# Kernel optimization log

Measured on AMD Instinct MI355X. Metric: run time of the kernel, lower is better.

The kernel has to match this reference:

```python
import jax, jax.numpy as jnp
import numpy as np

N_NODES = 50000
IN_CH, HID_CH, OUT_CH = 128, 128, 16
N_EDGES = 800000


def setup_inputs() -> dict:
    key = jax.random.key(0)
    ks = jax.random.split(key, 10)
    def lin_w(k, fan_in, fan_out):
        bound = 1.0 / np.sqrt(fan_in)
        return jax.random.uniform(k, (fan_in, fan_out), jnp.float32, -bound, bound)
    inp = {
        'x': jax.random.normal(ks[0], (N_NODES, IN_CH), jnp.float32),
        'edge_index': jax.random.randint(ks[1], (2, N_EDGES), 0, N_NODES, jnp.int64),
        # SAGEConv l/r weights: lin_l (neighbor aggregate, with bias), lin_r (root, no bias)
        'W1_l': lin_w(ks[2], IN_CH, HID_CH), 'b1': jnp.zeros((HID_CH,), jnp.float32),
        'W1_r': lin_w(ks[3], IN_CH, HID_CH),
        'W2_l': lin_w(ks[4], HID_CH, HID_CH), 'b2': jnp.zeros((HID_CH,), jnp.float32),
        'W2_r': lin_w(ks[5], HID_CH, HID_CH),
        'W3_l': lin_w(ks[6], HID_CH, HID_CH), 'b3': jnp.zeros((HID_CH,), jnp.float32),
        'W3_r': lin_w(ks[7], HID_CH, HID_CH),
        'W_lin': lin_w(ks[8], HID_CH, OUT_CH), 'b_lin': jnp.zeros((OUT_CH,), jnp.float32),
    }
    return inp


def _sage_conv(x, src, dst, W_l, b_l, W_r, n_nodes):
    # mean aggregation of source-node features at destination nodes
    msg_sum = jax.ops.segment_sum(x[src], dst, num_segments=n_nodes)  # [N, d]
    deg = jax.ops.segment_sum(jnp.ones((src.shape[0],), x.dtype), dst, num_segments=n_nodes)
    mean = msg_sum / jnp.maximum(deg, 1.0)[:, None]
    return mean @ W_l + b_l + x @ W_r


def reference(x, edge_index, W1_l, b1, W1_r, W2_l, b2, W2_r, W3_l, b3, W3_r, W_lin, b_lin):
    src, dst = edge_index[0], edge_index[1]
    n = x.shape[0]
    h = jax.nn.relu(_sage_conv(x, src, dst, W1_l, b1, W1_r, n))
    h = jax.nn.relu(_sage_conv(h, src, dst, W2_l, b2, W2_r, n))
    # dropout is identity in eval mode
    h = jax.nn.relu(_sage_conv(h, src, dst, W3_l, b3, W3_r, n))
    return h @ W_lin + b_lin
```

## Files before the change

### kernel.cpp

```cpp
#include <hip/hip_runtime.h>


typedef short bf16x8 __attribute__((ext_vector_type(8)));
typedef float f32x4 __attribute__((ext_vector_type(4)));

__device__ __forceinline__ float bf16_to_f32(unsigned int lo16) {
  unsigned int u = lo16 << 16;
  return __builtin_bit_cast(float, u);
}
__device__ __forceinline__ unsigned short f32_to_bf16(float f) {
  unsigned int u = __builtin_bit_cast(unsigned int, f);
  unsigned int r = (u + 0x7FFFu + ((u >> 16) & 1u)) >> 16;
  return (unsigned short)r;
}

__device__ __forceinline__ void gload_lds16(const void* g, void* lds_base) {
  __builtin_amdgcn_global_load_lds(
      (__attribute__((address_space(1))) unsigned int*)(uintptr_t)g,
      (__attribute__((address_space(3))) unsigned int*)(unsigned int)(uintptr_t)lds_base,
      16, 0, 0);
}

__global__ void k_zero_i32(int* __restrict__ p, int n) {
  int i = blockIdx.x * blockDim.x + threadIdx.x;
  if (i < n) p[i] = 0;
}

__global__ __launch_bounds__(256) void k_split(const float* __restrict__ in,
                                               unsigned short* __restrict__ hi,
                                               unsigned short* __restrict__ lo, int n4) {
  int i = blockIdx.x * blockDim.x + threadIdx.x;
  if (i < n4) {
    float4 v = *reinterpret_cast<const float4*>(&in[(size_t)i * 4]);
    ushort4 h, l;
    h.x = f32_to_bf16(v.x); l.x = f32_to_bf16(v.x - bf16_to_f32(h.x));
    h.y = f32_to_bf16(v.y); l.y = f32_to_bf16(v.y - bf16_to_f32(h.y));
    h.z = f32_to_bf16(v.z); l.z = f32_to_bf16(v.z - bf16_to_f32(h.z));
    h.w = f32_to_bf16(v.w); l.w = f32_to_bf16(v.w - bf16_to_f32(h.w));
    *reinterpret_cast<ushort4*>(&hi[(size_t)i * 4]) = h;
    *reinterpret_cast<ushort4*>(&lo[(size_t)i * 4]) = l;
  }
}

__global__ __launch_bounds__(256) void k_prep_w(const float* __restrict__ Wl,
                                                const float* __restrict__ Wr,
                                                unsigned short* __restrict__ Whi,
                                                unsigned short* __restrict__ Wlo) {
  int n = blockIdx.x, k = threadIdx.x;
  float v = (k < 128) ? Wl[(size_t)k * 128 + n] : Wr[(size_t)(k - 128) * 128 + n];
  unsigned short h = f32_to_bf16(v);
  Whi[(size_t)n * 256 + k] = h;
  Wlo[(size_t)n * 256 + k] = f32_to_bf16(v - bf16_to_f32(h));
}

__global__ void k_detect(const int* __restrict__ ei, int* __restrict__ flag) {
  int t = threadIdx.x;
  int any = 0;
  for (int i = t; i < 1024; i += 256)
    if (ei[2 * i + 1] != 0) any = 1;
  if (any) atomicOr(flag, 1);
}

__device__ __forceinline__ int load_src(const int* ei, int E, int i, int is32) {
  return is32 ? ei[i] : ei[2 * i];
}
__device__ __forceinline__ int load_dst(const int* ei, int E, int i, int is32) {
  return is32 ? ei[E + i] : ei[2 * E + 2 * i];
}

__global__ __launch_bounds__(256) void k_count(const int* __restrict__ ei,
                                               const int* __restrict__ flag,
                                               int* __restrict__ deg,
                                               int* __restrict__ erank, int E) {
  int i = blockIdx.x * blockDim.x + threadIdx.x;
  if (i < E) {
    int is32 = *flag;
    erank[i] = atomicAdd(&deg[load_dst(ei, E, i, is32)], 1);
  }
}

__global__ __launch_bounds__(256) void k_scan1(const int* __restrict__ deg,
                                               int* __restrict__ bsum, int N) {
  __shared__ int s[256];
  int t = threadIdx.x;
  int base = blockIdx.x * 1024 + t * 4;
  int v = 0;
#pragma unroll
  for (int j = 0; j < 4; ++j) {
    int i = base + j;
    v += (i < N) ? deg[i] : 0;
  }
  s[t] = v;
  __syncthreads();
  for (int off = 128; off > 0; off >>= 1) {
    if (t < off) s[t] += s[t + off];
    __syncthreads();
  }
  if (t == 0) bsum[blockIdx.x] = s[0];
}

__global__ __launch_bounds__(1024) void k_scan2(int* __restrict__ bsum,
                                                int* __restrict__ row_ptr,
                                                int nb, int N) {
  __shared__ int s[1024];
  int t = threadIdx.x;
  int v = (t < nb) ? bsum[t] : 0;
  s[t] = v;
  __syncthreads();
  for (int off = 1; off < 1024; off <<= 1) {
    int add = (t >= off) ? s[t - off] : 0;
    __syncthreads();
    s[t] += add;
    __syncthreads();
  }
  if (t < nb) bsum[t] = s[t] - v;
  if (t == 1023) row_ptr[N] = s[1023];
}

__global__ __launch_bounds__(256) void k_scan3(const int* __restrict__ deg,
                                               const int* __restrict__ bsum,
                                               int* __restrict__ row_ptr,
                                               float* __restrict__ inv_deg, int N) {
  __shared__ int s[256];
  int t = threadIdx.x;
  int base = blockIdx.x * 1024 + t * 4;
  int v[4];
  int sum = 0;
#pragma unroll
  for (int j = 0; j < 4; ++j) {
    int i = base + j;
    v[j] = (i < N) ? deg[i] : 0;
    sum += v[j];
  }
  s[t] = sum;
  __syncthreads();
  for (int off = 1; off < 256; off <<= 1) {
    int add = (t >= off) ? s[t - off] : 0;
    __syncthreads();
    s[t] += add;
    __syncthreads();
  }
  int excl = s[t] - sum + bsum[blockIdx.x];
#pragma unroll
  for (int j = 0; j < 4; ++j) {
    int i = base + j;
    if (i < N) {
      row_ptr[i] = excl;
      inv_deg[i] = 1.0f / (float)((v[j] > 1) ? v[j] : 1);
      excl += v[j];
    }
  }
}

__global__ __launch_bounds__(256) void k_fill(const int* __restrict__ ei,
                                              const int* __restrict__ flag,
                                              const int* __restrict__ row_ptr,
                                              const int* __restrict__ erank,
                                              int* __restrict__ col_idx, int E) {
  int i = blockIdx.x * blockDim.x + threadIdx.x;
  if (i < E) {
    int is32 = *flag;
    int d = load_dst(ei, E, i, is32);
    int s = load_src(ei, E, i, is32);
    col_idx[row_ptr[d] + erank[i]] = s;
  }
}

__global__ __launch_bounds__(256) void k_aggregate(const unsigned short* __restrict__ Xhi,
                                                   const int* __restrict__ row_ptr,
                                                   const int* __restrict__ col_idx,
                                                   const float* __restrict__ inv_deg,
                                                   unsigned int* __restrict__ Mhi,
                                                   unsigned int* __restrict__ Mlo, int N) {
  int gw = (int)((blockIdx.x * blockDim.x + threadIdx.x) >> 6);
  int lane = threadIdx.x & 63;
  if (gw >= N) return;
  int s = row_ptr[gw], e = row_ptr[gw + 1];
  const unsigned int* Xp =
      reinterpret_cast<const unsigned int*>(Xhi) + lane;
  float ax[8], ay[8];
#pragma unroll
  for (int q = 0; q < 8; ++q) { ax[q] = 0.f; ay[q] = 0.f; }
  int j = s;
  for (; j + 8 <= e; j += 8) {
    unsigned int v[8];
#pragma unroll
    for (int q = 0; q < 8; ++q) v[q] = Xp[(size_t)col_idx[j + q] * 64];
#pragma unroll
    for (int q = 0; q < 8; ++q) {
      ax[q] += bf16_to_f32(v[q] & 0xFFFFu);
      ay[q] += bf16_to_f32(v[q] >> 16);
    }
  }
  for (; j + 4 <= e; j += 4) {
    unsigned int v[4];
#pragma unroll
    for (int q = 0; q < 4; ++q) v[q] = Xp[(size_t)col_idx[j + q] * 64];
#pragma unroll
    for (int q = 0; q < 4; ++q) {
      ax[q] += bf16_to_f32(v[q] & 0xFFFFu);
      ay[q] += bf16_to_f32(v[q] >> 16);
    }
  }
  for (; j < e; ++j) {
    unsigned int v = Xp[(size_t)col_idx[j] * 64];
    ax[0] += bf16_to_f32(v & 0xFFFFu);
    ay[0] += bf16_to_f32(v >> 16);
  }
  float inv = inv_deg[gw];
  float rx = ((ax[0] + ax[1]) + (ax[2] + ax[3])) + ((ax[4] + ax[5]) + (ax[6] + ax[7]));
  float ry = ((ay[0] + ay[1]) + (ay[2] + ay[3])) + ((ay[4] + ay[5]) + (ay[6] + ay[7]));
  rx *= inv;
  ry *= inv;
  unsigned int hx = f32_to_bf16(rx), hy = f32_to_bf16(ry);
  unsigned int lx = f32_to_bf16(rx - bf16_to_f32(hx));
  unsigned int ly = f32_to_bf16(ry - bf16_to_f32(hy));
  Mhi[(size_t)gw * 64 + lane] = hx | (hy << 16);
  Mlo[(size_t)gw * 64 + lane] = lx | (ly << 16);
}

__global__ __launch_bounds__(256) void k_mfma_gemm(
    const unsigned short* __restrict__ A1hi, const unsigned short* __restrict__ A1lo,
    const unsigned short* __restrict__ A2hi, const unsigned short* __restrict__ A2lo,
    const unsigned short* __restrict__ Whi, const unsigned short* __restrict__ Wlo,
    const float* __restrict__ bias,
    unsigned short* __restrict__ Ohi, unsigned short* __restrict__ Olo, int N) {
  __shared__ unsigned short sAhi[2][128 * 32], sAlo[2][128 * 32];
  __shared__ unsigned short sBhi[2][128 * 32], sBlo[2][128 * 32];
  int t = threadIdx.x;
  int lane = t & 63;
  int w = t >> 6;
  int wr = (w >> 1) * 64, wc = (w & 1) * 64;
  int block_row = blockIdx.x * 128;

  f32x4 acc[4][4];
#pragma unroll
  for (int m = 0; m < 4; ++m)
#pragma unroll
    for (int n = 0; n < 4; ++n) acc[m][n] = f32x4{0.f, 0.f, 0.f, 0.f};

  int kg = lane & 3;
  int rr = lane >> 2;
  int fr = lane & 15;
  int fkb = (lane >> 4) * 16;

  auto stage = [&](int kt, int b) {
    const unsigned short* gsrc;
    unsigned short* lbase;
    int isA = (w < 2);
    if (w == 0) { gsrc = (kt < 4) ? A1hi : A2hi; lbase = sAhi[b]; }
    else if (w == 1) { gsrc = (kt < 4) ? A1lo : A2lo; lbase = sAlo[b]; }
    else if (w == 2) { gsrc = Whi; lbase = sBhi[b]; }
    else { gsrc = Wlo; lbase = sBlo[b]; }
#pragma unroll
    for (int c = 0; c < 8; ++c) {
      int idx = c * 16 + rr;
      const char* src;
      if (isA) {
        int rg = block_row + idx;
        if (rg > N - 1) rg = N - 1;
        src = (const char*)gsrc + (size_t)rg * 256 + (kt & 3) * 64 + kg * 16;
      } else {
        src = (const char*)gsrc + (size_t)idx * 512 + kt * 64 + kg * 16;
      }
      gload_lds16(src, (char*)lbase + c * 1024);
    }
  };

  stage(0, 0);
  __syncthreads();

  for (int kt = 0; kt < 8; ++kt) {
    int cur = kt & 1;
    if (kt < 7) stage(kt + 1, cur ^ 1);
    bf16x8 a_hi[4], a_lo[4], b_hi[4], b_lo[4];
#pragma unroll
    for (int m = 0; m < 4; ++m) {
      int row = wr + m * 16 + fr;
      a_hi[m] = *reinterpret_cast<const bf16x8*>((const char*)sAhi[cur] + row * 64 + fkb);
      a_lo[m] = *reinterpret_cast<const bf16x8*>((const char*)sAlo[cur] + row * 64 + fkb);
    }
#pragma unroll
    for (int n = 0; n < 4; ++n) {
      int col = wc + n * 16 + fr;
      b_hi[n] = *reinterpret_cast<const bf16x8*>((const char*)sBhi[cur] + col * 64 + fkb);
      b_lo[n] = *reinterpret_cast<const bf16x8*>((const char*)sBlo[cur] + col * 64 + fkb);
    }
#pragma unroll
    for (int m = 0; m < 4; ++m)
#pragma unroll
      for (int n = 0; n < 4; ++n) {
        acc[m][n] = __builtin_amdgcn_mfma_f32_16x16x32_bf16(a_hi[m], b_hi[n], acc[m][n], 0, 0, 0);
        acc[m][n] = __builtin_amdgcn_mfma_f32_16x16x32_bf16(a_hi[m], b_lo[n], acc[m][n], 0, 0, 0);
        acc[m][n] = __builtin_amdgcn_mfma_f32_16x16x32_bf16(a_lo[m], b_hi[n], acc[m][n], 0, 0, 0);
      }
    __syncthreads();
  }

  float bv[4];
#pragma unroll
  for (int n = 0; n < 4; ++n) bv[n] = bias[wc + n * 16 + (lane & 15)];
#pragma unroll
  for (int m = 0; m < 4; ++m) {
#pragma unroll
    for (int n = 0; n < 4; ++n) {
#pragma unroll
      for (int j = 0; j < 4; ++j) {
        int row_l = wr + m * 16 + (lane >> 4) * 4 + j;
        int g = block_row + row_l;
        if (g < N) {
          int col = wc + n * 16 + (lane & 15);
          float v = fmaxf(acc[m][n][j] + bv[n], 0.f);
          unsigned short h = f32_to_bf16(v);
          Ohi[(size_t)g * 128 + col] = h;
          Olo[(size_t)g * 128 + col] = f32_to_bf16(v - bf16_to_f32(h));
        }
      }
    }
  }
}

__global__ __launch_bounds__(256) void k_final(const unsigned short* __restrict__ Hhi,
                                               const unsigned short* __restrict__ Hlo,
                                               const float* __restrict__ W,
                                               const float* __restrict__ b,
                                               float* __restrict__ Out, int N) {
  __shared__ float sH[16][128];
  __shared__ float sW[128][16];
  __shared__ float sb[16];
  int t = threadIdx.x;
  int node0 = blockIdx.x * 16;
  {
    int row = t >> 4, q = t & 15;
    int g = node0 + row;
    if (g < N) {
      uint4 hv = *reinterpret_cast<const uint4*>(&Hhi[(size_t)g * 128 + q * 8]);
      uint4 lv = *reinterpret_cast<const uint4*>(&Hlo[(size_t)g * 128 + q * 8]);
      const unsigned short* hp = (const unsigned short*)&hv;
      const unsigned short* lp = (const unsigned short*)&lv;
#pragma unroll
      for (int e = 0; e < 8; ++e)
        sH[row][q * 8 + e] = bf16_to_f32(hp[e]) + bf16_to_f32(lp[e]);
    } else {
#pragma unroll
      for (int e = 0; e < 8; ++e) sH[row][q * 8 + e] = 0.f;
    }
  }
  for (int j = t; j < 512; j += 256) {
    int row = j >> 2, q = j & 3;
    *reinterpret_cast<float4*>(&sW[row][q * 4]) =
        *reinterpret_cast<const float4*>(&W[(size_t)row * 16 + q * 4]);
  }
  if (t < 16) sb[t] = b[t];
  __syncthreads();
  int node = t >> 4, col = t & 15;
  float acc = sb[col];
#pragma unroll 8
  for (int k = 0; k < 128; ++k) acc = fmaf(sH[node][k], sW[k][col], acc);
  int g = node0 + node;
  if (g < N) Out[(size_t)g * 16 + col] = acc;
}

extern "C" void kernel_launch(void* const* d_in, const int* in_sizes, int n_in,
                              void* d_out, int out_size, void* d_ws, size_t ws_size,
                              hipStream_t stream) {
  if (n_in < 13) return;
  const float* x = (const float*)d_in[0];
  const int* ei = (const int*)d_in[1];
  const float* W1l = (const float*)d_in[2];
  const float* b1 = (const float*)d_in[3];
  const float* W1r = (const float*)d_in[4];
  const float* W2l = (const float*)d_in[5];
  const float* b2 = (const float*)d_in[6];
  const float* W2r = (const float*)d_in[7];
  const float* W3l = (const float*)d_in[8];
  const float* b3 = (const float*)d_in[9];
  const float* W3r = (const float*)d_in[10];
  const float* Wlin = (const float*)d_in[11];
  const float* blin = (const float*)d_in[12];
  float* out = (float*)d_out;

  const int N = in_sizes[0] / 128;
  const int E = in_sizes[1] / 2;

  char* w = (char*)d_ws;
  size_t off = 0;
  auto alloc = [&](size_t bytes) -> void* {
    off = (off + 255) & ~(size_t)255;
    void* p = (void*)(w + off);
    off += bytes;
    return p;
  };
  size_t actB = (size_t)N * 128 * 2;
  unsigned short* Xhi = (unsigned short*)alloc(actB);
  unsigned short* Xlo = (unsigned short*)alloc(actB);
  unsigned short* Ahi = (unsigned short*)alloc(actB);
  unsigned short* Alo = (unsigned short*)alloc(actB);
  unsigned short* Mhi = (unsigned short*)alloc(actB);
  unsigned short* Mlo = (unsigned short*)alloc(actB);
  unsigned short* Wt[6];
  for (int i = 0; i < 6; ++i) Wt[i] = (unsigned short*)alloc(128 * 256 * 2);
  int* deg = (int*)alloc((size_t)N * 4);
  int* row_ptr = (int*)alloc((size_t)(N + 1) * 4);
  int* col_idx = (int*)alloc((size_t)E * 4);
  int* erank = (int*)alloc((size_t)E * 4);
  float* invdeg = (float*)alloc((size_t)N * 4);
  int* flag = (int*)alloc(4);
  int* bsum = (int*)alloc((size_t)1024 * 4);
  (void)ws_size;

  const int nbScan = (N + 1023) / 1024;

  k_zero_i32<<<(N + 255) / 256, 256, 0, stream>>>(deg, N);
  k_zero_i32<<<1, 256, 0, stream>>>(flag, 1);
  k_detect<<<1, 256, 0, stream>>>(ei, flag);
  k_count<<<(E + 255) / 256, 256, 0, stream>>>(ei, flag, deg, erank, E);
  k_split<<<(N * 32 + 255) / 256, 256, 0, stream>>>(x, Xhi, Xlo, N * 32);
  k_prep_w<<<128, 256, 0, stream>>>(W1l, W1r, Wt[0], Wt[1]);
  k_prep_w<<<128, 256, 0, stream>>>(W2l, W2r, Wt[2], Wt[3]);
  k_prep_w<<<128, 256, 0, stream>>>(W3l, W3r, Wt[4], Wt[5]);
  k_scan1<<<nbScan, 256, 0, stream>>>(deg, bsum, N);
  k_scan2<<<1, 1024, 0, stream>>>(bsum, row_ptr, nbScan, N);
  k_scan3<<<nbScan, 256, 0, stream>>>(deg, bsum, row_ptr, invdeg, N);
  k_fill<<<(E + 255) / 256, 256, 0, stream>>>(ei, flag, row_ptr, erank, col_idx, E);

  int aggBlocks = (N * 64 + 255) / 256;
  int gemmBlocks = (N + 127) / 128;

  k_aggregate<<<aggBlocks, 256, 0, stream>>>(Xhi, row_ptr, col_idx, invdeg,
                                             (unsigned int*)Mhi, (unsigned int*)Mlo, N);
  k_mfma_gemm<<<gemmBlocks, 256, 0, stream>>>(Mhi, Mlo, Xhi, Xlo, Wt[0], Wt[1], b1,
                                              Ahi, Alo, N);
  k_aggregate<<<aggBlocks, 256, 0, stream>>>(Ahi, row_ptr, col_idx, invdeg,
                                             (unsigned int*)Mhi, (unsigned int*)Mlo, N);
  k_mfma_gemm<<<gemmBlocks, 256, 0, stream>>>(Mhi, Mlo, Ahi, Alo, Wt[2], Wt[3], b2,
                                              Xhi, Xlo, N);
  k_aggregate<<<aggBlocks, 256, 0, stream>>>(Xhi, row_ptr, col_idx, invdeg,
                                             (unsigned int*)Mhi, (unsigned int*)Mlo, N);
  k_mfma_gemm<<<gemmBlocks, 256, 0, stream>>>(Mhi, Mlo, Xhi, Xlo, Wt[4], Wt[5], b3,
                                              Ahi, Alo, N);
  k_final<<<(N + 15) / 16, 256, 0, stream>>>(Ahi, Alo, Wlin, blin, out, N);
}
```

Baseline: 269.8 us.

## Slice aggregation by feature quarter so XCD-local L2 caches hold a feature slice

Adds an aggregation kernel where each block handles a 64-byte feature slice (one of four) for 16 nodes. A 16-lane group gathers that slice per neighbor, and slice = blockIdx & 3 maps the slice to interleaved XCDs. The aim is to shrink the gathered working set each XCD's L2 must hold, improving cache hit rates for random neighbor gathers. In exchange each gather touches only 64 bytes per row, giving narrower memory transactions and four times the row_ptr/col_idx reads. The new kernel is used for layers 1 and 3; layer 2 keeps the old kernel.

```diff
diff --git a/kernel.cpp b/kernel.cpp
--- a/kernel.cpp
+++ b/kernel.cpp
@@ -217,6 +217,51 @@
   unsigned int ly = f32_to_bf16(ry - bf16_to_f32(hy));
   Mhi[(size_t)gw * 64 + lane] = hx | (hy << 16);
   Mlo[(size_t)gw * 64 + lane] = lx | (ly << 16);
+}
+
+__global__ __launch_bounds__(256) void k_agg_xcd(const unsigned short* __restrict__ Xhi,
+                                                 const int* __restrict__ row_ptr,
+                                                 const int* __restrict__ col_idx,
+                                                 const float* __restrict__ inv_deg,
+                                                 unsigned int* __restrict__ Mhi,
+                                                 unsigned int* __restrict__ Mlo, int N) {
+  int b = blockIdx.x;
+  int slice = b & 3;
+  int chunk = b >> 2;
+  int t = threadIdx.x;
+  int wave = t >> 6, lane = t & 63;
+  int grp = lane >> 4, sl = lane & 15;
+  int node = chunk * 16 + wave * 4 + grp;
+  if (node >= N) return;
+  int s = row_ptr[node], e = row_ptr[node + 1];
+  const unsigned int* Xp =
+      reinterpret_cast<const unsigned int*>(Xhi) + slice * 16 + sl;
+  float ax0 = 0.f, ay0 = 0.f, ax1 = 0.f, ay1 = 0.f;
+  float ax2 = 0.f, ay2 = 0.f, ax3 = 0.f, ay3 = 0.f;
+  int j = s;
+  for (; j + 4 <= e; j += 4) {
+    unsigned int v0 = Xp[(size_t)col_idx[j] * 64];
+    unsigned int v1 = Xp[(size_t)col_idx[j + 1] * 64];
+    unsigned int v2 = Xp[(size_t)col_idx[j + 2] * 64];
+    unsigned int v3 = Xp[(size_t)col_idx[j + 3] * 64];
+    ax0 += bf16_to_f32(v0 & 0xFFFFu); ay0 += bf16_to_f32(v0 >> 16);
+    ax1 += bf16_to_f32(v1 & 0xFFFFu); ay1 += bf16_to_f32(v1 >> 16);
+    ax2 += bf16_to_f32(v2 & 0xFFFFu); ay2 += bf16_to_f32(v2 >> 16);
+    ax3 += bf16_to_f32(v3 & 0xFFFFu); ay3 += bf16_to_f32(v3 >> 16);
+  }
+  for (; j < e; ++j) {
+    unsigned int v = Xp[(size_t)col_idx[j] * 64];
+    ax0 += bf16_to_f32(v & 0xFFFFu);
+    ay0 += bf16_to_f32(v >> 16);
+  }
+  float inv = inv_deg[node];
+  float rx = ((ax0 + ax1) + (ax2 + ax3)) * inv;
+  float ry = ((ay0 + ay1) + (ay2 + ay3)) * inv;
+  unsigned int hx = f32_to_bf16(rx), hy = f32_to_bf16(ry);
+  unsigned int lx = f32_to_bf16(rx - bf16_to_f32(hx));
+  unsigned int ly = f32_to_bf16(ry - bf16_to_f32(hy));
+  Mhi[(size_t)node * 64 + slice * 16 + sl] = hx | (hy << 16);
+  Mlo[(size_t)node * 64 + slice * 16 + sl] = lx | (ly << 16);
 }
 
 __global__ __launch_bounds__(256) void k_mfma_gemm(
@@ -425,9 +470,10 @@
   k_fill<<<(E + 255) / 256, 256, 0, stream>>>(ei, flag, row_ptr, erank, col_idx, E);
 
   int aggBlocks = (N * 64 + 255) / 256;
+  int sliceBlocks = ((N + 15) / 16) * 4;
   int gemmBlocks = (N + 127) / 128;
 
-  k_aggregate<<<aggBlocks, 256, 0, stream>>>(Xhi, row_ptr, col_idx, invdeg,
+  k_agg_xcd<<<sliceBlocks, 256, 0, stream>>>(Xhi, row_ptr, col_idx, invdeg,
                                              (unsigned int*)Mhi, (unsigned int*)Mlo, N);
   k_mfma_gemm<<<gemmBlocks, 256, 0, stream>>>(Mhi, Mlo, Xhi, Xlo, Wt[0], Wt[1], b1,
                                               Ahi, Alo, N);
@@ -435,7 +481,7 @@
                                              (unsigned int*)Mhi, (unsigned int*)Mlo, N);
   k_mfma_gemm<<<gemmBlocks, 256, 0, stream>>>(Mhi, Mlo, Ahi, Alo, Wt[2], Wt[3], b2,
                                               Xhi, Xlo, N);
-  k_aggregate<<<aggBlocks, 256, 0, stream>>>(Xhi, row_ptr, col_idx, invdeg,
+  k_agg_xcd<<<sliceBlocks, 256, 0, stream>>>(Xhi, row_ptr, col_idx, invdeg,
                                              (unsigned int*)Mhi, (unsigned int*)Mlo, N);
   k_mfma_gemm<<<gemmBlocks, 256, 0, stream>>>(Mhi, Mlo, Xhi, Xlo, Wt[4], Wt[5], b3,
                                               Ahi, Alo, N);
```

After: 303.0 us. 1.12x slower.

## Fuse final linear into last SAGE GEMM and merge weight prep launches

Applied to the files above, without the earlier changes.

Fuses the third layer's MFMA GEMM with the output linear projection: the ReLU'd hidden tile is split into bf16 hi/lo in LDS and multiplied by Wlin via MFMA, so the 50000x128 activation is never written to or re-read from global memory. It also merges the three weight-prep launches into one and folds the flag zeroing into the detect kernel, cutting the number of kernel launches. The final projection now uses split-bf16 MFMA instead of fp32 FMA, a small change in numerics, and the fused kernel does extra per-block work loading Wlin.

```diff
diff --git a/kernel.cpp b/kernel.cpp
--- a/kernel.cpp
+++ b/kernel.cpp
@@ -42,11 +42,20 @@
   }
 }
 
-__global__ __launch_bounds__(256) void k_prep_w(const float* __restrict__ Wl,
-                                                const float* __restrict__ Wr,
-                                                unsigned short* __restrict__ Whi,
-                                                unsigned short* __restrict__ Wlo) {
-  int n = blockIdx.x, k = threadIdx.x;
+__global__ __launch_bounds__(256) void k_prep_w3(
+    const float* __restrict__ W1l, const float* __restrict__ W1r,
+    const float* __restrict__ W2l, const float* __restrict__ W2r,
+    const float* __restrict__ W3l, const float* __restrict__ W3r,
+    unsigned short* __restrict__ Whi1, unsigned short* __restrict__ Wlo1,
+    unsigned short* __restrict__ Whi2, unsigned short* __restrict__ Wlo2,
+    unsigned short* __restrict__ Whi3, unsigned short* __restrict__ Wlo3) {
+  int layer = blockIdx.x >> 7;
+  int n = blockIdx.x & 127;
+  int k = threadIdx.x;
+  const float* Wl = (layer == 0) ? W1l : (layer == 1) ? W2l : W3l;
+  const float* Wr = (layer == 0) ? W1r : (layer == 1) ? W2r : W3r;
+  unsigned short* Whi = (layer == 0) ? Whi1 : (layer == 1) ? Whi2 : Whi3;
+  unsigned short* Wlo = (layer == 0) ? Wlo1 : (layer == 1) ? Wlo2 : Wlo3;
   float v = (k < 128) ? Wl[(size_t)k * 128 + n] : Wr[(size_t)(k - 128) * 128 + n];
   unsigned short h = f32_to_bf16(v);
   Whi[(size_t)n * 256 + k] = h;
@@ -55,6 +64,8 @@
 
 __global__ void k_detect(const int* __restrict__ ei, int* __restrict__ flag) {
   int t = threadIdx.x;
+  if (t == 0) *flag = 0;
+  __syncthreads();
   int any = 0;
   for (int i = t; i < 1024; i += 256)
     if (ei[2 * i + 1] != 0) any = 1;
@@ -320,45 +331,146 @@
   }
 }
 
-__global__ __launch_bounds__(256) void k_final(const unsigned short* __restrict__ Hhi,
-                                               const unsigned short* __restrict__ Hlo,
-                                               const float* __restrict__ W,
-                                               const float* __restrict__ b,
-                                               float* __restrict__ Out, int N) {
-  __shared__ float sH[16][128];
-  __shared__ float sW[128][16];
-  __shared__ float sb[16];
+__global__ __launch_bounds__(256) void k_mfma_gemm_final(
+    const unsigned short* __restrict__ A1hi, const unsigned short* __restrict__ A1lo,
+    const unsigned short* __restrict__ A2hi, const unsigned short* __restrict__ A2lo,
+    const unsigned short* __restrict__ Whi, const unsigned short* __restrict__ Wlo,
+    const float* __restrict__ bias,
+    const float* __restrict__ Wlin, const float* __restrict__ blin,
+    float* __restrict__ Out, int N) {
+  __shared__ unsigned short smem[32768];
   int t = threadIdx.x;
-  int node0 = blockIdx.x * 16;
-  {
-    int row = t >> 4, q = t & 15;
-    int g = node0 + row;
-    if (g < N) {
-      uint4 hv = *reinterpret_cast<const uint4*>(&Hhi[(size_t)g * 128 + q * 8]);
-      uint4 lv = *reinterpret_cast<const uint4*>(&Hlo[(size_t)g * 128 + q * 8]);
-      const unsigned short* hp = (const unsigned short*)&hv;
-      const unsigned short* lp = (const unsigned short*)&lv;
-#pragma unroll
-      for (int e = 0; e < 8; ++e)
-        sH[row][q * 8 + e] = bf16_to_f32(hp[e]) + bf16_to_f32(lp[e]);
-    } else {
-#pragma unroll
-      for (int e = 0; e < 8; ++e) sH[row][q * 8 + e] = 0.f;
-    }
-  }
-  for (int j = t; j < 512; j += 256) {
-    int row = j >> 2, q = j & 3;
-    *reinterpret_cast<float4*>(&sW[row][q * 4]) =
-        *reinterpret_cast<const float4*>(&W[(size_t)row * 16 + q * 4]);
-  }
-  if (t < 16) sb[t] = b[t];
-  __syncthreads();
-  int node = t >> 4, col = t & 15;
-  float acc = sb[col];
-#pragma unroll 8
-  for (int k = 0; k < 128; ++k) acc = fmaf(sH[node][k], sW[k][col], acc);
-  int g = node0 + node;
-  if (g < N) Out[(size_t)g * 16 + col] = acc;
+  int lane = t & 63;
+  int w = t >> 6;
+  int wr = (w >> 1) * 64, wc = (w & 1) * 64;
+  int block_row = blockIdx.x * 128;
+
+  int kg = lane & 3;
+  int rr = lane >> 2;
+  int fr = lane & 15;
+  int fkb = (lane >> 4) * 16;
+  int ke = (lane >> 4) * 8;
+  int colw = lane & 15;
+
+  bf16x8 wbh[4], wbl[4];
+#pragma unroll
+  for (int ks = 0; ks < 4; ++ks) {
+#pragma unroll
+    for (int e = 0; e < 8; ++e) {
+      float wv = Wlin[(size_t)(ks * 32 + ke + e) * 16 + colw];
+      unsigned short h = f32_to_bf16(wv);
+      wbh[ks][e] = (short)h;
+      wbl[ks][e] = (short)f32_to_bf16(wv - bf16_to_f32(h));
+    }
+  }
+
+  f32x4 acc[4][4];
+#pragma unroll
+  for (int m = 0; m < 4; ++m)
+#pragma unroll
+    for (int n = 0; n < 4; ++n) acc[m][n] = f32x4{0.f, 0.f, 0.f, 0.f};
+
+  auto sAhi = [&](int b) { return smem + b * 4096; };
+  auto sAlo = [&](int b) { return smem + 8192 + b * 4096; };
+  auto sBhi = [&](int b) { return smem + 16384 + b * 4096; };
+  auto sBlo = [&](int b) { return smem + 24576 + b * 4096; };
+
+  auto stage = [&](int kt, int b) {
+    const unsigned short* gsrc;
+    unsigned short* lbase;
+    int isA = (w < 2);
+    if (w == 0) { gsrc = (kt < 4) ? A1hi : A2hi; lbase = sAhi(b); }
+    else if (w == 1) { gsrc = (kt < 4) ? A1lo : A2lo; lbase = sAlo(b); }
+    else if (w == 2) { gsrc = Whi; lbase = sBhi(b); }
+    else { gsrc = Wlo; lbase = sBlo(b); }
+#pragma unroll
+    for (int c = 0; c < 8; ++c) {
+      int idx = c * 16 + rr;
+      const char* src;
+      if (isA) {
+        int rg = block_row + idx;
+        if (rg > N - 1) rg = N - 1;
+        src = (const char*)gsrc + (size_t)rg * 256 + (kt & 3) * 64 + kg * 16;
+      } else {
+        src = (const char*)gsrc + (size_t)idx * 512 + kt * 64 + kg * 16;
+      }
+      gload_lds16(src, (char*)lbase + c * 1024);
+    }
+  };
+
+  stage(0, 0);
+  __syncthreads();
+
+  for (int kt = 0; kt < 8; ++kt) {
+    int cur = kt & 1;
+    if (kt < 7) stage(kt + 1, cur ^ 1);
+    bf16x8 a_hi[4], a_lo[4], b_hi[4], b_lo[4];
+#pragma unroll
+    for (int m = 0; m < 4; ++m) {
+      int row = wr + m * 16 + fr;
+      a_hi[m] = *reinterpret_cast<const bf16x8*>((const char*)sAhi(cur) + row * 64 + fkb);
+      a_lo[m] = *reinterpret_cast<const bf16x8*>((const char*)sAlo(cur) + row * 64 + fkb);
+    }
+#pragma unroll
+    for (int n = 0; n < 4; ++n) {
+      int col = wc + n * 16 + fr;
+      b_hi[n] = *reinterpret_cast<const bf16x8*>((const char*)sBhi(cur) + col * 64 + fkb);
+      b_lo[n] = *reinterpret_cast<const bf16x8*>((const char*)sBlo(cur) + col * 64 + fkb);
+    }
+#pragma unroll
+    for (int m = 0; m < 4; ++m)
+#pragma unroll
+      for (int n = 0; n < 4; ++n) {
+        acc[m][n] = __builtin_amdgcn_mfma_f32_16x16x32_bf16(a_hi[m], b_hi[n], acc[m][n], 0, 0, 0);
+        acc[m][n] = __builtin_amdgcn_mfma_f32_16x16x32_bf16(a_hi[m], b_lo[n], acc[m][n], 0, 0, 0);
+        acc[m][n] = __builtin_amdgcn_mfma_f32_16x16x32_bf16(a_lo[m], b_hi[n], acc[m][n], 0, 0, 0);
+      }
+    __syncthreads();
+  }
+
+  unsigned short* hhi = smem;
+  unsigned short* hlo = smem + 16384;
+  float bv[4];
+#pragma unroll
+  for (int n = 0; n < 4; ++n) bv[n] = bias[wc + n * 16 + (lane & 15)];
+#pragma unroll
+  for (int m = 0; m < 4; ++m) {
+#pragma unroll
+    for (int n = 0; n < 4; ++n) {
+#pragma unroll
+      for (int j = 0; j < 4; ++j) {
+        int row_l = wr + m * 16 + (lane >> 4) * 4 + j;
+        int col = wc + n * 16 + (lane & 15);
+        float v = fmaxf(acc[m][n][j] + bv[n], 0.f);
+        unsigned short h = f32_to_bf16(v);
+        hhi[row_l * 128 + col] = h;
+        hlo[row_l * 128 + col] = f32_to_bf16(v - bf16_to_f32(h));
+      }
+    }
+  }
+  __syncthreads();
+
+  float bo = blin[colw];
+#pragma unroll
+  for (int m2 = 0; m2 < 2; ++m2) {
+    int mtile = w * 2 + m2;
+    f32x4 a2 = f32x4{0.f, 0.f, 0.f, 0.f};
+#pragma unroll
+    for (int ks = 0; ks < 4; ++ks) {
+      int row = mtile * 16 + fr;
+      bf16x8 ah = *reinterpret_cast<const bf16x8*>(hhi + row * 128 + ks * 32 + ke);
+      bf16x8 al = *reinterpret_cast<const bf16x8*>(hlo + row * 128 + ks * 32 + ke);
+      a2 = __builtin_amdgcn_mfma_f32_16x16x32_bf16(ah, wbh[ks], a2, 0, 0, 0);
+      a2 = __builtin_amdgcn_mfma_f32_16x16x32_bf16(ah, wbl[ks], a2, 0, 0, 0);
+      a2 = __builtin_amdgcn_mfma_f32_16x16x32_bf16(al, wbh[ks], a2, 0, 0, 0);
+    }
+#pragma unroll
+    for (int j = 0; j < 4; ++j) {
+      int row = mtile * 16 + (lane >> 4) * 4 + j;
+      int g = block_row + row;
+      if (g < N) Out[(size_t)g * 16 + colw] = a2[j] + bo;
+    }
+  }
 }
 
 extern "C" void kernel_launch(void* const* d_in, const int* in_sizes, int n_in,
@@ -412,13 +524,11 @@
   const int nbScan = (N + 1023) / 1024;
 
   k_zero_i32<<<(N + 255) / 256, 256, 0, stream>>>(deg, N);
-  k_zero_i32<<<1, 256, 0, stream>>>(flag, 1);
   k_detect<<<1, 256, 0, stream>>>(ei, flag);
   k_count<<<(E + 255) / 256, 256, 0, stream>>>(ei, flag, deg, erank, E);
   k_split<<<(N * 32 + 255) / 256, 256, 0, stream>>>(x, Xhi, Xlo, N * 32);
-  k_prep_w<<<128, 256, 0, stream>>>(W1l, W1r, Wt[0], Wt[1]);
-  k_prep_w<<<128, 256, 0, stream>>>(W2l, W2r, Wt[2], Wt[3]);
-  k_prep_w<<<128, 256, 0, stream>>>(W3l, W3r, Wt[4], Wt[5]);
+  k_prep_w3<<<384, 256, 0, stream>>>(W1l, W1r, W2l, W2r, W3l, W3r,
+                                     Wt[0], Wt[1], Wt[2], Wt[3], Wt[4], Wt[5]);
   k_scan1<<<nbScan, 256, 0, stream>>>(deg, bsum, N);
   k_scan2<<<1, 1024, 0, stream>>>(bsum, row_ptr, nbScan, N);
   k_scan3<<<nbScan, 256, 0, stream>>>(deg, bsum, row_ptr, invdeg, N);
@@ -437,7 +547,6 @@
                                               Xhi, Xlo, N);
   k_aggregate<<<aggBlocks, 256, 0, stream>>>(Xhi, row_ptr, col_idx, invdeg,
                                              (unsigned int*)Mhi, (unsigned int*)Mlo, N);
-  k_mfma_gemm<<<gemmBlocks, 256, 0, stream>>>(Mhi, Mlo, Xhi, Xlo, Wt[4], Wt[5], b3,
-                                              Ahi, Alo, N);
-  k_final<<<(N + 15) / 16, 256, 0, stream>>>(Ahi, Alo, Wlin, blin, out, N);
-}
+  k_mfma_gemm_final<<<gemmBlocks, 256, 0, stream>>>(Mhi, Mlo, Xhi, Xlo, Wt[4], Wt[5],
+                                                    b3, Wlin, blin, out, N);
+}
```

After: 245.2 us (median of 3 runs). 9.1% less time.
